# Optimization experiments

Hardware: AMD Instinct MI355X
Metric: run time of the kernel (lower is better)

## Reference

```python
import jax, jax.numpy as jnp
import numpy as np

D = 256; H = 4; DK = 32; DV = D // H; DFF = 1024
NTF = 600; NG = 8000
EPS = 1e-5


def layer_norm(x, g, b):
    m = jnp.mean(x, -1, keepdims=True)
    v = jnp.mean((x - m) ** 2, -1, keepdims=True)
    return (x - m) / jnp.sqrt(v + EPS) * g + b


def setup_inputs() -> dict:
    key = jax.random.key(0)
    ks = jax.random.split(key, 32)
    def nrm(i, shape, s=1.0):
        return jax.random.normal(ks[i], shape, dtype=jnp.float32) * s
    w = 0.02  # init scale for weights
    inp = {
        "H_TF": nrm(0, (NTF, D)),
        "H_G": nrm(1, (NG, D)),
        "z_exp": nrm(2, (NG, D)),
        "z_seq": nrm(3, (NG, D)),
        "z_txt": nrm(4, (NG, D)),
        "tf_idx": jax.random.randint(ks[5], (NTF,), 0, NG),
        "WQ_seq": nrm(6, (H * DK, D), w), "WK_seq": nrm(7, (H * DK, D), w),
        "WQ_exp": nrm(8, (H * DK, D), w), "WK_exp": nrm(9, (H * DK, D), w),
        "WQ_txt": nrm(10, (H * DK, D), w), "WK_txt": nrm(11, (H * DK, D), w),
        "gate_w": jnp.broadcast_to(jnp.eye(3, dtype=jnp.float32), (H, 3, 3)),
        "gate_b": jnp.zeros((H, 3), jnp.float32),
        "WVG": nrm(12, (D, D), w), "WVTF": nrm(13, (D, D), w),
        "WOTF": nrm(14, (D, D), w), "WOG": nrm(15, (D, D), w),
        "ln_atf_g": jnp.ones((D,), jnp.float32), "ln_atf_b": jnp.zeros((D,), jnp.float32),
        "ln_ag_g": jnp.ones((D,), jnp.float32), "ln_ag_b": jnp.zeros((D,), jnp.float32),
        "ln_ftf_g": jnp.ones((D,), jnp.float32), "ln_ftf_b": jnp.zeros((D,), jnp.float32),
        "ln_fg_g": jnp.ones((D,), jnp.float32), "ln_fg_b": jnp.zeros((D,), jnp.float32),
        "ftf_W1": nrm(16, (DFF, D), w), "ftf_b1": jnp.zeros((DFF,), jnp.float32),
        "ftf_W2": nrm(17, (D, DFF), w), "ftf_b2": jnp.zeros((D,), jnp.float32),
        "fg_W1": nrm(18, (DFF, D), w), "fg_b1": jnp.zeros((DFF,), jnp.float32),
        "fg_W2": nrm(19, (D, DFF), w), "fg_b2": jnp.zeros((D,), jnp.float32),
    }
    return inp


def reference(H_TF, H_G, z_exp, z_seq, z_txt, tf_idx,
              WQ_seq, WK_seq, WQ_exp, WK_exp, WQ_txt, WK_txt,
              gate_w, gate_b, WVG, WVTF, WOTF, WOG,
              ln_atf_g, ln_atf_b, ln_ag_g, ln_ag_b,
              ln_ftf_g, ln_ftf_b, ln_fg_g, ln_fg_b,
              ftf_W1, ftf_b1, ftf_W2, ftf_b2,
              fg_W1, fg_b1, fg_W2, fg_b2):
    n_tf, n_gene = H_TF.shape[0], H_G.shape[0]
    scale = float(DK) ** 0.5

    H_TF_n = layer_norm(H_TF, ln_atf_g, ln_atf_b)
    H_G_n = layer_norm(H_G, ln_ag_g, ln_ag_b)

    z_seq_tf = z_seq[tf_idx]; z_exp_tf = z_exp[tf_idx]; z_txt_tf = z_txt[tf_idx]
    Q_seq = (z_seq_tf @ WQ_seq.T).reshape(n_tf, H, DK)
    K_seq = (z_seq @ WK_seq.T).reshape(n_gene, H, DK)
    Q_exp = (z_exp_tf @ WQ_exp.T).reshape(n_tf, H, DK)
    K_exp = (z_exp @ WK_exp.T).reshape(n_gene, H, DK)
    Q_txt = (z_txt_tf @ WQ_txt.T).reshape(n_tf, H, DK)
    K_txt = (z_txt @ WK_txt.T).reshape(n_gene, H, DK)

    s_bind = jnp.einsum('thd,ghd->htg', Q_seq, K_seq) / scale
    s_coexpr = jnp.einsum('thd,ghd->htg', Q_exp, K_exp) / scale
    s_know = jnp.einsum('thd,ghd->htg', Q_txt, K_txt) / scale

    # evidence gate: per-(head,tf,gene) softmax mixture over the 3 evidence channels
    s = jnp.stack([s_bind, s_coexpr, s_know], axis=-1)            # [H, t, g, 3]
    logits = jnp.einsum('htge,hef->htgf', s, gate_w) + gate_b[:, None, None, :]
    alpha = jax.nn.softmax(logits, axis=-1)                        # [H, t, g, 3]
    u = jnp.einsum('htge,htge->htg', alpha, s)                     # gated mixture
    A = jax.nn.softmax(u, axis=-1)                                 # softmax over genes

    V_G = (H_G_n @ WVG.T).reshape(n_gene, H, DV)
    V_TF = (H_TF_n @ WVTF.T).reshape(n_tf, H, DV)
    out_tf = jnp.einsum('htg,ghv->thv', A, V_G).reshape(n_tf, D) @ WOTF.T
    out_g = jnp.einsum('htg,thv->ghv', A, V_TF).reshape(n_gene, D) @ WOG.T

    H_TF2 = H_TF + out_tf
    H_G2 = H_G + out_g

    x = layer_norm(H_TF2, ln_ftf_g, ln_ftf_b)
    H_TF3 = H_TF2 + jax.nn.gelu(x @ ftf_W1.T + ftf_b1, approximate=False) @ ftf_W2.T + ftf_b2
    y = layer_norm(H_G2, ln_fg_g, ln_fg_b)
    H_G3 = H_G2 + jax.nn.gelu(y @ fg_W1.T + fg_b1, approximate=False) @ fg_W2.T + fg_b2

    return (H_TF3, H_G3, A.mean(0), u.mean(0), alpha.mean(0))
```

## Files before the change

kernel.cpp:

```cpp
#include <hip/hip_runtime.h>
#include <hip/hip_bf16.h>

#define NTF 600
#define NG  8000
#define DD  256
#define HH  4
#define DKK 32
#define DVV 64
#define DFF 1024

typedef __attribute__((ext_vector_type(8))) short frag_ab;
typedef __attribute__((ext_vector_type(4))) float frag_cd;

__device__ __forceinline__ unsigned short f2bu(float f) {
    __hip_bfloat16 h = __float2bfloat16(f);
    return __builtin_bit_cast(unsigned short, h);
}
__device__ __forceinline__ short f2bs(float f) { return (short)f2bu(f); }

__global__ __launch_bounds__(256)
void cvt3_kernel(const float* __restrict__ a, const float* __restrict__ b, const float* __restrict__ c,
                 unsigned short* __restrict__ oa, unsigned short* __restrict__ ob,
                 unsigned short* __restrict__ oc, int n4) {
    for (int i = blockIdx.x * 256 + threadIdx.x; i < 3 * n4; i += gridDim.x * 256) {
        int sel = i / n4, j = i - sel * n4;
        const float* src = (sel == 0) ? a : (sel == 1) ? b : c;
        unsigned short* dst = (sel == 0) ? oa : (sel == 1) ? ob : oc;
        float4 v = ((const float4*)src)[j];
        ushort4 o = {f2bu(v.x), f2bu(v.y), f2bu(v.z), f2bu(v.w)};
        ((ushort4*)dst)[j] = o;
    }
}

__global__ __launch_bounds__(256)
void cvt_w_kernel(const float* s0, const float* s1, const float* s2, const float* s3,
                  const float* s4, const float* s5, const float* s6, const float* s7,
                  const float* s8, const float* s9, const float* s10, const float* s11,
                  const float* s12, unsigned short* __restrict__ dst) {
    const int y = blockIdx.y;
    const float* src; int off, n;
    switch (y) {
        case 0:  src = s0;  off = 0;       n = 32768;  break;
        case 1:  src = s1;  off = 32768;   n = 32768;  break;
        case 2:  src = s2;  off = 65536;   n = 32768;  break;
        case 3:  src = s3;  off = 98304;   n = 32768;  break;
        case 4:  src = s4;  off = 131072;  n = 32768;  break;
        case 5:  src = s5;  off = 163840;  n = 32768;  break;
        case 6:  src = s6;  off = 196608;  n = 65536;  break;
        case 7:  src = s7;  off = 262144;  n = 65536;  break;
        case 8:  src = s8;  off = 327680;  n = 65536;  break;
        case 9:  src = s9;  off = 393216;  n = 262144; break;
        case 10: src = s10; off = 655360;  n = 262144; break;
        case 11: src = s11; off = 917504;  n = 262144; break;
        default: src = s12; off = 1179648; n = 262144; break;
    }
    const int n4 = n >> 2;
    for (int i = blockIdx.x * 256 + threadIdx.x; i < n4; i += gridDim.x * 256) {
        float4 v = ((const float4*)src)[i];
        ushort4 o = {f2bu(v.x), f2bu(v.y), f2bu(v.z), f2bu(v.w)};
        ((ushort4*)(dst + off))[i] = o;
    }
}

__global__ __launch_bounds__(64)
void ln_b_kernel(const float* __restrict__ x, const float* __restrict__ g,
                 const float* __restrict__ b, unsigned short* __restrict__ y) {
    int row = blockIdx.x;
    int tid = threadIdx.x;
    const float4* xp = (const float4*)(x + (size_t)row * DD);
    float4 v = xp[tid];
    float s = v.x + v.y + v.z + v.w;
    #pragma unroll
    for (int off = 32; off > 0; off >>= 1) s += __shfl_xor(s, off, 64);
    float mean = s * (1.f / 256.f);
    float dx = v.x - mean, dy = v.y - mean, dz = v.z - mean, dw = v.w - mean;
    float q = dx*dx + dy*dy + dz*dz + dw*dw;
    #pragma unroll
    for (int off = 32; off > 0; off >>= 1) q += __shfl_xor(q, off, 64);
    float inv = rsqrtf(q * (1.f / 256.f) + 1e-5f);
    float4 gg = ((const float4*)g)[tid];
    float4 bb = ((const float4*)b)[tid];
    ushort4 o = {f2bu(dx * inv * gg.x + bb.x), f2bu(dy * inv * gg.y + bb.y),
                 f2bu(dz * inv * gg.z + bb.z), f2bu(dw * inv * gg.w + bb.w)};
    ((ushort4*)(y + (size_t)row * DD))[tid] = o;
}

__global__ __launch_bounds__(256)
void gather_b_kernel(const float* __restrict__ zs, const float* __restrict__ ze,
                     const float* __restrict__ zt, const int* __restrict__ idx,
                     unsigned short* __restrict__ os, unsigned short* __restrict__ oe,
                     unsigned short* __restrict__ ot) {
    int t = blockIdx.x, j = threadIdx.x;
    size_t src = (size_t)idx[t] * DD + j;
    size_t dst = (size_t)t * DD + j;
    os[dst] = f2bu(zs[src]);
    oe[dst] = f2bu(ze[src]);
    ot[dst] = f2bu(zt[src]);
}

template<bool XF32, bool BIAS, bool GELU, bool RES, bool OB16>
__device__ __forceinline__
void mgemm_core(const void* __restrict__ Xv, const unsigned short* __restrict__ W,
                const float* __restrict__ bias, const float* __restrict__ res,
                void* __restrict__ Yv, int M, int N, int K) {
    const int lane = threadIdx.x & 63, wv = threadIdx.x >> 6;
    const int wm = wv >> 1, wn = wv & 1;
    const int lr = lane & 15, lk = lane >> 4;
    const int m0 = blockIdx.x * 64, n0 = blockIdx.y * 128;
    frag_cd zz = {0.f, 0.f, 0.f, 0.f};
    frag_cd acc[2][4];
    #pragma unroll
    for (int mi = 0; mi < 2; ++mi)
        #pragma unroll
        for (int ni = 0; ni < 4; ++ni) acc[mi][ni] = zz;
    int arow[2], brow[4];
    #pragma unroll
    for (int mi = 0; mi < 2; ++mi) arow[mi] = min(m0 + wm * 32 + mi * 16 + lr, M - 1);
    #pragma unroll
    for (int ni = 0; ni < 4; ++ni) brow[ni] = n0 + wn * 64 + ni * 16 + lr;
    for (int k0 = 0; k0 < K; k0 += 32) {
        frag_ab af[2], bfr[4];
        #pragma unroll
        for (int mi = 0; mi < 2; ++mi) {
            if (XF32) {
                const float* xp = (const float*)Xv + (size_t)arow[mi] * K + k0 + lk * 8;
                float4 v0 = *(const float4*)xp;
                float4 v1 = *(const float4*)(xp + 4);
                frag_ab t;
                t[0] = f2bs(v0.x); t[1] = f2bs(v0.y); t[2] = f2bs(v0.z); t[3] = f2bs(v0.w);
                t[4] = f2bs(v1.x); t[5] = f2bs(v1.y); t[6] = f2bs(v1.z); t[7] = f2bs(v1.w);
                af[mi] = t;
            } else {
                af[mi] = *(const frag_ab*)((const unsigned short*)Xv + (size_t)arow[mi] * K + k0 + lk * 8);
            }
        }
        #pragma unroll
        for (int ni = 0; ni < 4; ++ni)
            bfr[ni] = *(const frag_ab*)(W + (size_t)brow[ni] * K + k0 + lk * 8);
        #pragma unroll
        for (int mi = 0; mi < 2; ++mi)
            #pragma unroll
            for (int ni = 0; ni < 4; ++ni)
                acc[mi][ni] = __builtin_amdgcn_mfma_f32_16x16x32_bf16(af[mi], bfr[ni], acc[mi][ni], 0, 0, 0);
    }
    #pragma unroll
    for (int ni = 0; ni < 4; ++ni) {
        const int n = brow[ni];
        const float bn = BIAS ? bias[n] : 0.f;
        #pragma unroll
        for (int mi = 0; mi < 2; ++mi) {
            #pragma unroll
            for (int r = 0; r < 4; ++r) {
                const int m = m0 + wm * 32 + mi * 16 + lk * 4 + r;
                if (m < M) {
                    float v = acc[mi][ni][r] + bn;
                    if (GELU) v = 0.5f * v * (1.f + erff(v * 0.70710678118654752f));
                    if (RES)  v += res[(size_t)m * N + n];
                    if (OB16) ((unsigned short*)Yv)[(size_t)m * N + n] = f2bu(v);
                    else      ((float*)Yv)[(size_t)m * N + n] = v;
                }
            }
        }
    }
}

template<bool XF32, bool BIAS, bool GELU, bool RES, bool OB16>
__global__ __launch_bounds__(256)
void mgemm_kernel(const void* __restrict__ X, const unsigned short* __restrict__ W,
                  const float* __restrict__ bias, const float* __restrict__ res,
                  void* __restrict__ Y, int M, int N, int K) {
    mgemm_core<XF32, BIAS, GELU, RES, OB16>(X, W, bias, res, Y, M, N, K);
}

__global__ __launch_bounds__(256)
void mgemm3_kernel(const unsigned short* X0, const unsigned short* W0, unsigned short* Y0,
                   const unsigned short* X1, const unsigned short* W1, unsigned short* Y1,
                   const unsigned short* X2, const unsigned short* W2, unsigned short* Y2,
                   int M, int N, int K) {
    const unsigned short* X = (blockIdx.z == 0) ? X0 : (blockIdx.z == 1) ? X1 : X2;
    const unsigned short* W = (blockIdx.z == 0) ? W0 : (blockIdx.z == 1) ? W1 : W2;
    unsigned short*       Y = (blockIdx.z == 0) ? Y0 : (blockIdx.z == 1) ? Y1 : Y2;
    mgemm_core<false, false, false, false, true>(X, W, nullptr, nullptr, Y, M, N, K);
}

__global__ __launch_bounds__(256)
void scores_mfma(const unsigned short* __restrict__ Qse, const unsigned short* __restrict__ Qex,
                 const unsigned short* __restrict__ Qtx,
                 const unsigned short* __restrict__ Kse, const unsigned short* __restrict__ Kex,
                 const unsigned short* __restrict__ Ktx,
                 const float* __restrict__ gw, const float* __restrict__ gb,
                 float* __restrict__ U, float* __restrict__ umean, float* __restrict__ amean) {
    const int lane = threadIdx.x & 63, wv = threadIdx.x >> 6;
    const int lr = lane & 15, lk = lane >> 4;
    const int t0 = blockIdx.x * 64 + wv * 16;
    const int g0 = blockIdx.y * 64;
    const int tq = min(t0 + lr, NTF - 1);
    frag_cd zz = {0.f, 0.f, 0.f, 0.f};

    frag_ab qf[3][4];
    #pragma unroll
    for (int h = 0; h < HH; ++h) {
        qf[0][h] = *(const frag_ab*)(Qse + (size_t)tq * 128 + h * DKK + lk * 8);
        qf[1][h] = *(const frag_ab*)(Qex + (size_t)tq * 128 + h * DKK + lk * 8);
        qf[2][h] = *(const frag_ab*)(Qtx + (size_t)tq * 128 + h * DKK + lk * 8);
    }
    float gwr[HH][3][3], gbr[HH][3];
    #pragma unroll
    for (int h = 0; h < HH; ++h) {
        #pragma unroll
        for (int e = 0; e < 3; ++e)
            #pragma unroll
            for (int f = 0; f < 3; ++f) gwr[h][e][f] = gw[h * 9 + e * 3 + f];
        #pragma unroll
        for (int f = 0; f < 3; ++f) gbr[h][f] = gb[h * 3 + f];
    }
    const float sc = 0.17677669529663687f;

    #pragma unroll
    for (int gi = 0; gi < 4; ++gi) {
        const int gg = g0 + gi * 16;
        const int gk = gg + lr;
        float us[4] = {0.f, 0.f, 0.f, 0.f};
        float a0s[4] = {0.f, 0.f, 0.f, 0.f};
        float a1s[4] = {0.f, 0.f, 0.f, 0.f};
        float a2s[4] = {0.f, 0.f, 0.f, 0.f};
        #pragma unroll
        for (int h = 0; h < HH; ++h) {
            frag_ab kf0 = *(const frag_ab*)(Kse + (size_t)gk * 128 + h * DKK + lk * 8);
            frag_ab kf1 = *(const frag_ab*)(Kex + (size_t)gk * 128 + h * DKK + lk * 8);
            frag_ab kf2 = *(const frag_ab*)(Ktx + (size_t)gk * 128 + h * DKK + lk * 8);
            frag_cd s0 = __builtin_amdgcn_mfma_f32_16x16x32_bf16(qf[0][h], kf0, zz, 0, 0, 0);
            frag_cd s1 = __builtin_amdgcn_mfma_f32_16x16x32_bf16(qf[1][h], kf1, zz, 0, 0, 0);
            frag_cd s2 = __builtin_amdgcn_mfma_f32_16x16x32_bf16(qf[2][h], kf2, zz, 0, 0, 0);
            #pragma unroll
            for (int r = 0; r < 4; ++r) {
                const int t = t0 + lk * 4 + r;
                float e0 = s0[r] * sc, e1 = s1[r] * sc, e2 = s2[r] * sc;
                float lg0 = e0 * gwr[h][0][0] + e1 * gwr[h][1][0] + e2 * gwr[h][2][0] + gbr[h][0];
                float lg1 = e0 * gwr[h][0][1] + e1 * gwr[h][1][1] + e2 * gwr[h][2][1] + gbr[h][1];
                float lg2 = e0 * gwr[h][0][2] + e1 * gwr[h][1][2] + e2 * gwr[h][2][2] + gbr[h][2];
                float mx = fmaxf(lg0, fmaxf(lg1, lg2));
                float x0 = __expf(lg0 - mx), x1 = __expf(lg1 - mx), x2 = __expf(lg2 - mx);
                float inv = 1.f / (x0 + x1 + x2);
                float a0 = x0 * inv, a1 = x1 * inv, a2 = x2 * inv;
                float u = a0 * e0 + a1 * e1 + a2 * e2;
                if (t < NTF) U[((size_t)h * NTF + t) * NG + gg + lr] = u;
                us[r] += u; a0s[r] += a0; a1s[r] += a1; a2s[r] += a2;
            }
        }
        #pragma unroll
        for (int r = 0; r < 4; ++r) {
            const int t = t0 + lk * 4 + r;
            if (t < NTF) {
                size_t p = (size_t)t * NG + gg + lr;
                umean[p] = us[r] * 0.25f;
                amean[p * 3 + 0] = a0s[r] * 0.25f;
                amean[p * 3 + 1] = a1s[r] * 0.25f;
                amean[p * 3 + 2] = a2s[r] * 0.25f;
            }
        }
    }
}

__global__ __launch_bounds__(512)
void softmax_amean_kernel(float* __restrict__ U, float* __restrict__ Am) {
    __shared__ float sred[8];
    const int t = blockIdx.x, tid = threadIdx.x;
    const int w = tid >> 6;
    float am[16] = {};
    for (int h = 0; h < HH; ++h) {
        float* p = U + ((size_t)h * NTF + t) * NG;
        float v[16];
        float mx = -1e30f;
        #pragma unroll
        for (int i = 0; i < 16; ++i) {
            int j = i * 512 + tid;
            v[i] = (j < NG) ? p[j] : -1e30f;
            mx = fmaxf(mx, v[i]);
        }
        #pragma unroll
        for (int off = 32; off > 0; off >>= 1) mx = fmaxf(mx, __shfl_xor(mx, off, 64));
        __syncthreads();
        if ((tid & 63) == 0) sred[w] = mx;
        __syncthreads();
        mx = sred[0];
        #pragma unroll
        for (int k = 1; k < 8; ++k) mx = fmaxf(mx, sred[k]);
        float sum = 0.f;
        #pragma unroll
        for (int i = 0; i < 16; ++i) {
            int j = i * 512 + tid;
            v[i] = (j < NG) ? __expf(v[i] - mx) : 0.f;
            sum += v[i];
        }
        #pragma unroll
        for (int off = 32; off > 0; off >>= 1) sum += __shfl_xor(sum, off, 64);
        __syncthreads();
        if ((tid & 63) == 0) sred[w] = sum;
        __syncthreads();
        float tot = 0.f;
        #pragma unroll
        for (int k = 0; k < 8; ++k) tot += sred[k];
        float inv = 1.f / tot;
        #pragma unroll
        for (int i = 0; i < 16; ++i) {
            int j = i * 512 + tid;
            float a = v[i] * inv;
            if (j < NG) p[j] = a;
            am[i] += a;
        }
    }
    #pragma unroll
    for (int i = 0; i < 16; ++i) {
        int j = i * 512 + tid;
        if (j < NG) Am[(size_t)t * NG + j] = am[i] * 0.25f;
    }
}

__global__ __launch_bounds__(256)
void vgt_kernel(const float* __restrict__ VG, unsigned short* __restrict__ VGT) {
    __shared__ float tile[64][65];
    const int g0 = blockIdx.x * 64;
    const int h  = blockIdx.y;
    const int tid = threadIdx.x;
    const int c = tid & 63, r0 = (tid >> 6) * 16;
    #pragma unroll
    for (int i = 0; i < 16; ++i)
        tile[r0 + i][c] = VG[(size_t)(g0 + r0 + i) * DD + h * DVV + c];
    __syncthreads();
    #pragma unroll
    for (int i = 0; i < 16; ++i)
        VGT[(size_t)(h * 64 + r0 + i) * NG + g0 + c] = f2bu(tile[c][r0 + i]);
}

__global__ __launch_bounds__(256)
void attn_tf_mfma(const float* __restrict__ A, const unsigned short* __restrict__ VGT,
                  float* __restrict__ AT) {
    const int lane = threadIdx.x & 63, wv = threadIdx.x >> 6;
    const int lr = lane & 15, lk = lane >> 4;
    const int t0 = blockIdx.x * 64 + wv * 16;
    const int h  = blockIdx.y;
    const int kbase = blockIdx.z * 512;
    const float* arow = A + (size_t)h * NTF * NG + (size_t)min(t0 + lr, NTF - 1) * NG;
    const unsigned short* Vh = VGT + (size_t)h * 64 * NG;
    frag_cd zz = {0.f, 0.f, 0.f, 0.f};
    frag_cd acc[4] = {zz, zz, zz, zz};
    const int kend = min(kbase + 512, NG);
    for (int k0 = kbase; k0 < kend; k0 += 32) {
        const float* ap = arow + k0 + lk * 8;
        float4 v0 = *(const float4*)ap;
        float4 v1 = *(const float4*)(ap + 4);
        frag_ab af;
        af[0] = f2bs(v0.x); af[1] = f2bs(v0.y); af[2] = f2bs(v0.z); af[3] = f2bs(v0.w);
        af[4] = f2bs(v1.x); af[5] = f2bs(v1.y); af[6] = f2bs(v1.z); af[7] = f2bs(v1.w);
        #pragma unroll
        for (int ni = 0; ni < 4; ++ni) {
            frag_ab bf = *(const frag_ab*)(Vh + (size_t)(ni * 16 + lr) * NG + k0 + lk * 8);
            acc[ni] = __builtin_amdgcn_mfma_f32_16x16x32_bf16(af, bf, acc[ni], 0, 0, 0);
        }
    }
    #pragma unroll
    for (int ni = 0; ni < 4; ++ni) {
        const int v = ni * 16 + lr;
        #pragma unroll
        for (int r = 0; r < 4; ++r) {
            const int t = t0 + lk * 4 + r;
            if (t < NTF)
                atomicAdd(&AT[(size_t)t * DD + h * DVV + v], acc[ni][r]);
        }
    }
}

__global__ __launch_bounds__(256)
void attn_g_kernel(const float* __restrict__ A, const float* __restrict__ VTF,
                   unsigned short* __restrict__ ATb) {
    __shared__ float As[16][68];
    __shared__ float Vs[16][68];
    const int tid = threadIdx.x;
    const int tx = tid & 15, ty = tid >> 4;
    const int g0 = blockIdx.x * 64;
    const int h  = blockIdx.y;
    const float* Ah = A + (size_t)h * NTF * NG;
    float acc[4][4] = {};
    for (int t0 = 0; t0 < NTF; t0 += 16) {
        __syncthreads();
        #pragma unroll
        for (int j = 0; j < 4; ++j) {
            int idx = j * 256 + tid;
            int m = idx & 63, k = idx >> 6;
            int t = t0 + k;
            As[k][m] = (t < NTF) ? Ah[(size_t)t * NG + g0 + m] : 0.f;
            Vs[k][m] = (t < NTF) ? VTF[(size_t)t * DD + h * DVV + m] : 0.f;
        }
        __syncthreads();
        #pragma unroll
        for (int k = 0; k < 16; ++k) {
            float4 a4 = *(const float4*)&As[k][ty * 4];
            float4 b4 = *(const float4*)&Vs[k][tx * 4];
            float a[4] = {a4.x, a4.y, a4.z, a4.w};
            float b[4] = {b4.x, b4.y, b4.z, b4.w};
            #pragma unroll
            for (int i = 0; i < 4; ++i)
                #pragma unroll
                for (int j = 0; j < 4; ++j)
                    acc[i][j] += a[i] * b[j];
        }
    }
    #pragma unroll
    for (int i = 0; i < 4; ++i) {
        ushort4 o = {f2bu(acc[i][0]), f2bu(acc[i][1]), f2bu(acc[i][2]), f2bu(acc[i][3])};
        *(ushort4*)&ATb[(size_t)(g0 + ty * 4 + i) * DD + h * DVV + tx * 4] = o;
    }
}

template<bool RES>
__global__ __launch_bounds__(256)
void gemm_xwt(const float* __restrict__ X, const float* __restrict__ W,
              const float* __restrict__ res, float* __restrict__ Y, int M, int N, int K) {
    __shared__ float Xs[16][132];
    __shared__ float Ws[16][132];
    const int tid = threadIdx.x;
    const int bm = blockIdx.x * 128, bn = blockIdx.y * 128;
    const int tx = tid & 15, ty = tid >> 4;
    float acc[8][8] = {};
    for (int k0 = 0; k0 < K; k0 += 16) {
        __syncthreads();
        #pragma unroll
        for (int j = 0; j < 8; ++j) {
            int idx = j * 256 + tid;
            int k = idx & 15, m = idx >> 4;
            Xs[k][m] = (bm + m < M) ? X[(size_t)(bm + m) * K + k0 + k] : 0.f;
            Ws[k][m] = W[(size_t)(bn + m) * K + k0 + k];
        }
        __syncthreads();
        #pragma unroll
        for (int k = 0; k < 16; ++k) {
            float4 a0 = *(const float4*)&Xs[k][ty * 8];
            float4 a1 = *(const float4*)&Xs[k][ty * 8 + 4];
            float4 b0 = *(const float4*)&Ws[k][tx * 8];
            float4 b1 = *(const float4*)&Ws[k][tx * 8 + 4];
            float a[8] = {a0.x,a0.y,a0.z,a0.w,a1.x,a1.y,a1.z,a1.w};
            float b[8] = {b0.x,b0.y,b0.z,b0.w,b1.x,b1.y,b1.z,b1.w};
            #pragma unroll
            for (int i = 0; i < 8; ++i)
                #pragma unroll
                for (int j = 0; j < 8; ++j)
                    acc[i][j] += a[i] * b[j];
        }
    }
    #pragma unroll
    for (int i = 0; i < 8; ++i) {
        int m = bm + ty * 8 + i;
        if (m >= M) continue;
        #pragma unroll
        for (int j = 0; j < 8; ++j) {
            int n = bn + tx * 8 + j;
            float v = acc[i][j];
            if (RES) v += res[(size_t)m * N + n];
            Y[(size_t)m * N + n] = v;
        }
    }
}

extern "C" void kernel_launch(void* const* d_in, const int* in_sizes, int n_in,
                              void* d_out, int out_size, void* d_ws, size_t ws_size,
                              hipStream_t stream) {
    (void)in_sizes; (void)n_in; (void)out_size; (void)ws_size;
    const float* H_TF   = (const float*)d_in[0];
    const float* H_G    = (const float*)d_in[1];
    const float* z_exp  = (const float*)d_in[2];
    const float* z_seq  = (const float*)d_in[3];
    const float* z_txt  = (const float*)d_in[4];
    const int*   tf_idx = (const int*)d_in[5];
    const float* WQ_seq = (const float*)d_in[6];
    const float* WK_seq = (const float*)d_in[7];
    const float* WQ_exp = (const float*)d_in[8];
    const float* WK_exp = (const float*)d_in[9];
    const float* WQ_txt = (const float*)d_in[10];
    const float* WK_txt = (const float*)d_in[11];
    const float* gate_w = (const float*)d_in[12];
    const float* gate_b = (const float*)d_in[13];
    const float* WVG    = (const float*)d_in[14];
    const float* WVTF   = (const float*)d_in[15];
    const float* WOTF   = (const float*)d_in[16];
    const float* WOG    = (const float*)d_in[17];
    const float* ln_atf_g = (const float*)d_in[18];
    const float* ln_atf_b = (const float*)d_in[19];
    const float* ln_ag_g  = (const float*)d_in[20];
    const float* ln_ag_b  = (const float*)d_in[21];
    const float* ln_ftf_g = (const float*)d_in[22];
    const float* ln_ftf_b = (const float*)d_in[23];
    const float* ln_fg_g  = (const float*)d_in[24];
    const float* ln_fg_b  = (const float*)d_in[25];
    const float* ftf_W1 = (const float*)d_in[26];
    const float* ftf_b1 = (const float*)d_in[27];
    const float* ftf_W2 = (const float*)d_in[28];
    const float* ftf_b2 = (const float*)d_in[29];
    const float* fg_W1  = (const float*)d_in[30];
    const float* fg_b1  = (const float*)d_in[31];
    const float* fg_W2  = (const float*)d_in[32];
    const float* fg_b2  = (const float*)d_in[33];

    float* out = (float*)d_out;
    float* out_HTF3  = out;
    float* out_HG3   = out + 153600;
    float* out_Amean = out + 2201600;
    float* out_umean = out + 7001600;
    float* out_amean = out + 11801600;

    float* ws = (float*)d_ws;
    float* U    = ws;
    float* VG   = ws + 19200000;
    float* VTF  = VG + 2048000;
    float* ATtf = VTF + 153600;
    float* HTF2 = ATtf + 153600;
    float* HG2  = HTF2 + 153600;
    float* G2 = U;
    float* G1 = U + 8192000;
    unsigned short* bws   = (unsigned short*)(ws + 23756800);
    unsigned short* Kb_se = bws;
    unsigned short* Kb_ex = bws + 1024000;
    unsigned short* Kb_tx = bws + 2048000;
    unsigned short* Qb_se = bws + 3072000;
    unsigned short* Qb_ex = bws + 3148800;
    unsigned short* Qb_tx = bws + 3225600;
    unsigned short* Wb    = bws + 3302400;
    unsigned short* HTFnb = bws + 4744192;
    unsigned short* HGnb  = bws + 4897792;
    unsigned short* VGT   = bws + 6945792;
    unsigned short* zb_se = (unsigned short*)U;
    unsigned short* zb_ex = zb_se + 2048000;
    unsigned short* zb_tx = zb_se + 4096000;
    unsigned short* ztb_se = zb_se + 6144000;
    unsigned short* ztb_ex = ztb_se + 153600;
    unsigned short* ztb_tx = ztb_se + 307200;
    unsigned short* ATgb = (unsigned short*)VG;

    unsigned short* WQse_b = Wb + 0;
    unsigned short* WQex_b = Wb + 32768;
    unsigned short* WQtx_b = Wb + 65536;
    unsigned short* WKse_b = Wb + 98304;
    unsigned short* WKex_b = Wb + 131072;
    unsigned short* WKtx_b = Wb + 163840;
    unsigned short* WVGb   = Wb + 196608;
    unsigned short* WVTFb  = Wb + 262144;
    unsigned short* WOGb   = Wb + 327680;
    unsigned short* ftfW1b = Wb + 393216;
    unsigned short* ftfW2b = Wb + 655360;
    unsigned short* fgW1b  = Wb + 917504;
    unsigned short* fgW2b  = Wb + 1179648;

    cvt3_kernel<<<750, 256, 0, stream>>>(z_seq, z_exp, z_txt, zb_se, zb_ex, zb_tx, 512000);
    cvt_w_kernel<<<dim3(64, 13), 256, 0, stream>>>(
        WQ_seq, WQ_exp, WQ_txt, WK_seq, WK_exp, WK_txt,
        WVG, WVTF, WOG, ftf_W1, ftf_W2, fg_W1, fg_W2, Wb);

    ln_b_kernel<<<NTF, 64, 0, stream>>>(H_TF, ln_atf_g, ln_atf_b, HTFnb);
    ln_b_kernel<<<NG,  64, 0, stream>>>(H_G,  ln_ag_g,  ln_ag_b,  HGnb);

    gather_b_kernel<<<NTF, 256, 0, stream>>>(z_seq, z_exp, z_txt, tf_idx, ztb_se, ztb_ex, ztb_tx);

    mgemm3_kernel<<<dim3(10, 1, 3), 256, 0, stream>>>(ztb_se, WQse_b, Qb_se,
                                                      ztb_ex, WQex_b, Qb_ex,
                                                      ztb_tx, WQtx_b, Qb_tx, NTF, 128, DD);
    mgemm3_kernel<<<dim3(125, 1, 3), 256, 0, stream>>>(zb_se, WKse_b, Kb_se,
                                                       zb_ex, WKex_b, Kb_ex,
                                                       zb_tx, WKtx_b, Kb_tx, NG, 128, DD);
    mgemm_kernel<false,false,false,false,false><<<dim3(125, 2), 256, 0, stream>>>(
        HGnb, WVGb, nullptr, nullptr, VG, NG, DD, DD);
    mgemm_kernel<false,false,false,false,false><<<dim3(10, 2), 256, 0, stream>>>(
        HTFnb, WVTFb, nullptr, nullptr, VTF, NTF, DD, DD);

    vgt_kernel<<<dim3(125, HH), 256, 0, stream>>>(VG, VGT);

    scores_mfma<<<dim3(10, 125), 256, 0, stream>>>(
        Qb_se, Qb_ex, Qb_tx, Kb_se, Kb_ex, Kb_tx, gate_w, gate_b, U, out_umean, out_amean);

    softmax_amean_kernel<<<NTF, 512, 0, stream>>>(U, out_Amean);

    hipMemsetAsync(ATtf, 0, (size_t)NTF * DD * sizeof(float), stream);
    attn_tf_mfma<<<dim3(10, HH, 16), 256, 0, stream>>>(U, VGT, ATtf);
    attn_g_kernel<<<dim3(NG / 64, HH), 256, 0, stream>>>(U, VTF, ATgb);

    gemm_xwt<true><<<dim3(5, 2), 256, 0, stream>>>(ATtf, WOTF, H_TF, HTF2, NTF, DD, DD);
    mgemm_kernel<false,false,false,true,false><<<dim3(125, 2), 256, 0, stream>>>(
        ATgb, WOGb, nullptr, H_G, HG2, NG, DD, DD);

    ln_b_kernel<<<NTF, 64, 0, stream>>>(HTF2, ln_ftf_g, ln_ftf_b, HTFnb);
    mgemm_kernel<false,true,true,false,false><<<dim3(10, 8), 256, 0, stream>>>(
        HTFnb, ftfW1b, ftf_b1, nullptr, G1, NTF, DFF, DD);
    mgemm_kernel<true,true,false,true,false><<<dim3(10, 2), 256, 0, stream>>>(
        G1, ftfW2b, ftf_b2, HTF2, out_HTF3, NTF, DD, DFF);

    ln_b_kernel<<<NG, 64, 0, stream>>>(HG2, ln_fg_g, ln_fg_b, HGnb);
    mgemm_kernel<false,true,true,false,false><<<dim3(125, 8), 256, 0, stream>>>(
        HGnb, fgW1b, fg_b1, nullptr, G2, NG, DFF, DD);
    mgemm_kernel<true,true,false,true,false><<<dim3(125, 2), 256, 0, stream>>>(
        G2, fgW2b, fg_b2, HG2, out_HG3, NG, DD, DFF);
}
```

Before: 658.4 us.

## Store attention probabilities as bf16 in place and split gene-side attention over TFs

The softmax kernel now writes the normalized attention probabilities as bf16 into the first half of each fp32 row slot. The two attention-value kernels read these bf16 values directly, which halves the bytes they load and removes per-element conversion in the MFMA path. The gene-side kernel is also split three ways along the TF dimension to expose more blocks, and it accumulates into an fp32 buffer with atomics. The added costs are a memset, atomic traffic, and a different input mode for the output projection GEMM.

```diff
diff --git a/kernel.cpp b/kernel.cpp
--- a/kernel.cpp
+++ b/kernel.cpp
@@ -17,6 +17,10 @@
     return __builtin_bit_cast(unsigned short, h);
 }
 __device__ __forceinline__ short f2bs(float f) { return (short)f2bu(f); }
+__device__ __forceinline__ float b2f(unsigned short u) {
+    unsigned x = (unsigned)u << 16;
+    return __builtin_bit_cast(float, x);
+}
 
 __global__ __launch_bounds__(256)
 void cvt3_kernel(const float* __restrict__ a, const float* __restrict__ b, const float* __restrict__ c,
@@ -270,6 +274,7 @@
     float am[16] = {};
     for (int h = 0; h < HH; ++h) {
         float* p = U + ((size_t)h * NTF + t) * NG;
+        unsigned short* pb = (unsigned short*)p;
         float v[16];
         float mx = -1e30f;
         #pragma unroll
@@ -306,7 +311,7 @@
         for (int i = 0; i < 16; ++i) {
             int j = i * 512 + tid;
             float a = v[i] * inv;
-            if (j < NG) p[j] = a;
+            if (j < NG) pb[j] = f2bu(a);
             am[i] += a;
         }
     }
@@ -334,25 +339,21 @@
 }
 
 __global__ __launch_bounds__(256)
-void attn_tf_mfma(const float* __restrict__ A, const unsigned short* __restrict__ VGT,
+void attn_tf_mfma(const unsigned short* __restrict__ Ab, const unsigned short* __restrict__ VGT,
                   float* __restrict__ AT) {
     const int lane = threadIdx.x & 63, wv = threadIdx.x >> 6;
     const int lr = lane & 15, lk = lane >> 4;
     const int t0 = blockIdx.x * 64 + wv * 16;
     const int h  = blockIdx.y;
     const int kbase = blockIdx.z * 512;
-    const float* arow = A + (size_t)h * NTF * NG + (size_t)min(t0 + lr, NTF - 1) * NG;
+    const unsigned short* arow =
+        Ab + (size_t)(h * NTF + min(t0 + lr, NTF - 1)) * NG * 2;
     const unsigned short* Vh = VGT + (size_t)h * 64 * NG;
     frag_cd zz = {0.f, 0.f, 0.f, 0.f};
     frag_cd acc[4] = {zz, zz, zz, zz};
     const int kend = min(kbase + 512, NG);
     for (int k0 = kbase; k0 < kend; k0 += 32) {
-        const float* ap = arow + k0 + lk * 8;
-        float4 v0 = *(const float4*)ap;
-        float4 v1 = *(const float4*)(ap + 4);
-        frag_ab af;
-        af[0] = f2bs(v0.x); af[1] = f2bs(v0.y); af[2] = f2bs(v0.z); af[3] = f2bs(v0.w);
-        af[4] = f2bs(v1.x); af[5] = f2bs(v1.y); af[6] = f2bs(v1.z); af[7] = f2bs(v1.w);
+        frag_ab af = *(const frag_ab*)(arow + k0 + lk * 8);
         #pragma unroll
         for (int ni = 0; ni < 4; ++ni) {
             frag_ab bf = *(const frag_ab*)(Vh + (size_t)(ni * 16 + lr) * NG + k0 + lk * 8);
@@ -372,25 +373,26 @@
 }
 
 __global__ __launch_bounds__(256)
-void attn_g_kernel(const float* __restrict__ A, const float* __restrict__ VTF,
-                   unsigned short* __restrict__ ATb) {
+void attn_g_split(const unsigned short* __restrict__ Ab, const float* __restrict__ VTF,
+                  float* __restrict__ ATg) {
     __shared__ float As[16][68];
     __shared__ float Vs[16][68];
     const int tid = threadIdx.x;
     const int tx = tid & 15, ty = tid >> 4;
     const int g0 = blockIdx.x * 64;
     const int h  = blockIdx.y;
-    const float* Ah = A + (size_t)h * NTF * NG;
+    const int ts = blockIdx.z * 200;
+    const int te = min(ts + 200, NTF);
     float acc[4][4] = {};
-    for (int t0 = 0; t0 < NTF; t0 += 16) {
+    for (int t0 = ts; t0 < te; t0 += 16) {
         __syncthreads();
         #pragma unroll
         for (int j = 0; j < 4; ++j) {
             int idx = j * 256 + tid;
             int m = idx & 63, k = idx >> 6;
             int t = t0 + k;
-            As[k][m] = (t < NTF) ? Ah[(size_t)t * NG + g0 + m] : 0.f;
-            Vs[k][m] = (t < NTF) ? VTF[(size_t)t * DD + h * DVV + m] : 0.f;
+            As[k][m] = (t < te) ? b2f(Ab[(size_t)(h * NTF + t) * NG * 2 + g0 + m]) : 0.f;
+            Vs[k][m] = (t < te) ? VTF[(size_t)t * DD + h * DVV + m] : 0.f;
         }
         __syncthreads();
         #pragma unroll
@@ -407,10 +409,10 @@
         }
     }
     #pragma unroll
-    for (int i = 0; i < 4; ++i) {
-        ushort4 o = {f2bu(acc[i][0]), f2bu(acc[i][1]), f2bu(acc[i][2]), f2bu(acc[i][3])};
-        *(ushort4*)&ATb[(size_t)(g0 + ty * 4 + i) * DD + h * DVV + tx * 4] = o;
-    }
+    for (int i = 0; i < 4; ++i)
+        #pragma unroll
+        for (int j = 0; j < 4; ++j)
+            atomicAdd(&ATg[(size_t)(g0 + ty * 4 + i) * DD + h * DVV + tx * 4 + j], acc[i][j]);
 }
 
 template<bool RES>
@@ -517,6 +519,7 @@
     float* HG2  = HTF2 + 153600;
     float* G2 = U;
     float* G1 = U + 8192000;
+    float* ATg = VG;
     unsigned short* bws   = (unsigned short*)(ws + 23756800);
     unsigned short* Kb_se = bws;
     unsigned short* Kb_ex = bws + 1024000;
@@ -534,7 +537,7 @@
     unsigned short* ztb_se = zb_se + 6144000;
     unsigned short* ztb_ex = ztb_se + 153600;
     unsigned short* ztb_tx = ztb_se + 307200;
-    unsigned short* ATgb = (unsigned short*)VG;
+    unsigned short* Ab = (unsigned short*)U;
 
     unsigned short* WQse_b = Wb + 0;
     unsigned short* WQex_b = Wb + 32768;
@@ -579,12 +582,13 @@
     softmax_amean_kernel<<<NTF, 512, 0, stream>>>(U, out_Amean);
 
     hipMemsetAsync(ATtf, 0, (size_t)NTF * DD * sizeof(float), stream);
-    attn_tf_mfma<<<dim3(10, HH, 16), 256, 0, stream>>>(U, VGT, ATtf);
-    attn_g_kernel<<<dim3(NG / 64, HH), 256, 0, stream>>>(U, VTF, ATgb);
+    hipMemsetAsync(ATg,  0, (size_t)NG  * DD * sizeof(float), stream);
+    attn_tf_mfma<<<dim3(10, HH, 16), 256, 0, stream>>>(Ab, VGT, ATtf);
+    attn_g_split<<<dim3(NG / 64, HH, 3), 256, 0, stream>>>(Ab, VTF, ATg);
 
     gemm_xwt<true><<<dim3(5, 2), 256, 0, stream>>>(ATtf, WOTF, H_TF, HTF2, NTF, DD, DD);
-    mgemm_kernel<false,false,false,true,false><<<dim3(125, 2), 256, 0, stream>>>(
-        ATgb, WOGb, nullptr, H_G, HG2, NG, DD, DD);
+    mgemm_kernel<true,false,false,true,false><<<dim3(125, 2), 256, 0, stream>>>(
+        ATg, WOGb, nullptr, H_G, HG2, NG, DD, DD);
 
     ln_b_kernel<<<NTF, 64, 0, stream>>>(HTF2, ln_ftf_g, ln_ftf_b, HTFnb);
     mgemm_kernel<false,true,true,false,false><<<dim3(10, 8), 256, 0, stream>>>(
```

Result: slower. 684.9 us (+4.0%).
